# Kernel optimization log

Measured on AMD Instinct MI355X. Metric: run time of the kernel, lower is better.

## Reference

```python
import jax, jax.numpy as jnp
import numpy as np

D = 256      # d_model
K = 8        # knn neighbors
Q = 2048     # num queries
N = 32768    # num superpoints
H = 8        # mamba heads (d_inner/head_dim)
HD = 64      # head_dim
ST = 64      # state_size
DIN = H * HD                 # 512, expand*d_model
CONV = DIN + 2 * ST          # 640
NPROJ = 2 * DIN + 2 * ST + H # 1160
HID = 1024   # ffn hidden
NL = 2       # ssm layers
KC = 4       # conv kernel


def _ln(x, eps=1e-5):
    m = x.mean(-1, keepdims=True)
    v = ((x - m) ** 2).mean(-1, keepdims=True)
    return (x - m) * jax.lax.rsqrt(v + eps)


def _silu(x):
    return x * jax.nn.sigmoid(x)


def _mamba2(x, Win, Wconv, bconv, A_log, Dh, dtb, rmsw, Wout):
    # x: [B, L, D]; faithful HF Mamba2Mixer recurrent form
    B, L, _ = x.shape
    proj = x @ Win.T  # [B,L,NPROJ]
    z, xBC, dt = jnp.split(proj, [DIN, DIN + CONV], axis=-1)
    # causal depthwise conv1d, kernel KC, left pad KC-1
    xp = jnp.pad(xBC, ((0, 0), (KC - 1, 0), (0, 0)))
    conv = sum(xp[:, j:j + L, :] * Wconv[:, j] for j in range(KC))
    xBC = _silu(conv + bconv)
    xs, Bm, Cm = jnp.split(xBC, [DIN, DIN + ST], axis=-1)
    dt = jax.nn.softplus(dt + dtb)  # [B,L,H]
    A = -jnp.exp(A_log)             # [H]
    xh = xs.reshape(B, L, H, HD)
    dA = jnp.exp(dt * A)            # [B,L,H]
    dBx = dt[..., None, None] * Bm[:, :, None, None, :] * xh[..., None]  # [B,L,H,HD,ST]

    def step(h, inp):
        dA_t, dBx_t, C_t = inp
        h = h * dA_t[..., None, None] + dBx_t
        y = jnp.einsum('bhds,bs->bhd', h, C_t)
        return h, y

    h0 = jnp.zeros((B, H, HD, ST), x.dtype)
    _, ys = jax.lax.scan(step, h0, (dA.transpose(1, 0, 2),
                                    dBx.transpose(1, 0, 2, 3, 4),
                                    Cm.transpose(1, 0, 2)))
    y = ys.transpose(1, 0, 2, 3) + Dh[None, None, :, None] * xh
    y = y.reshape(B, L, DIN) * _silu(z)  # gated RMSNorm
    y = y * jax.lax.rsqrt((y * y).mean(-1, keepdims=True) + 1e-5) * rmsw
    return y @ Wout.T


def setup_inputs() -> dict:
    key = jax.random.key(0)
    ks = jax.random.split(key, 32)
    s = 0.02
    rn = lambda i, sh: jax.random.normal(ks[i], sh, jnp.float32) * s
    inp = {
        'query': jax.random.normal(ks[0], (Q, D), jnp.float32),
        'query_pos': jax.random.uniform(ks[1], (Q, 3), jnp.float32),
        'inst_feats': jax.random.normal(ks[2], (N, D), jnp.float32),
        'sp_coords': jax.random.uniform(ks[3], (N, 3), jnp.float32),
        'w_q': rn(4, (D, D)), 'w_v': rn(5, (D, D)), 'w_o': rn(6, (D, D)),
        'w_k': rn(7, (K, D)), 'w_b': jnp.zeros((K,), jnp.float32),
        'ssm_Win': rn(8, (NL, NPROJ, D)),
        'ssm_Wconv': rn(9, (NL, CONV, KC)),
        'ssm_bconv': jnp.zeros((NL, CONV), jnp.float32),
        'ssm_Alog': jnp.log(jnp.broadcast_to(jnp.arange(1, H + 1, dtype=jnp.float32), (NL, H))),
        'ssm_D': jnp.ones((NL, H), jnp.float32),
        'ssm_dtb': jax.random.uniform(ks[10], (NL, H), jnp.float32) * 0.1,
        'ssm_rmsw': jnp.ones((NL, DIN), jnp.float32),
        'ssm_Wout': rn(11, (NL, D, DIN)),
        'ffn_w1': rn(12, (HID, D)), 'ffn_b1': jnp.zeros((HID,), jnp.float32),
        'ffn_w2': rn(13, (D, HID)), 'ffn_b2': jnp.zeros((D,), jnp.float32),
        'order': jnp.stack([jax.random.permutation(ks[14], Q),
                            jax.random.permutation(ks[15], Q)]).astype(jnp.int32),
    }
    return inp


def reference(query, query_pos, inst_feats, sp_coords,
              w_q, w_v, w_o, w_k, w_b,
              ssm_Win, ssm_Wconv, ssm_bconv, ssm_Alog, ssm_D, ssm_dtb, ssm_rmsw, ssm_Wout,
              ffn_w1, ffn_b1, ffn_w2, ffn_b2, order):
    # --- MambaAggregation: KNN group + small-K softmax mixing ---
    d2 = (query_pos ** 2).sum(-1, keepdims=True) + (sp_coords ** 2).sum(-1)[None, :] \
         - 2.0 * query_pos @ sp_coords.T  # [Q,N]
    _, idx = jax.lax.top_k(-d2, K)        # [Q,K] nearest neighbors
    feat = inst_feats[idx]                # [Q,K,D]
    q = query @ w_q.T
    v = feat @ w_v.T
    kw = jax.nn.softmax(q @ w_k.T + w_b, axis=-1)          # [Q,K]
    w = jnp.einsum('qk,qd,qkd->qd', kw, q, v)
    x = _ln(w @ w_o.T + query)

    # --- SSM: serialize along 2 orders, Mamba2 mix, unsort, average ---
    inv = jnp.argsort(order, axis=1)  # [2,Q]
    for l in range(NL):
        sc = x
        xn = _ln(x)
        xs = xn[order]  # [2,Q,D], two serialization paths as batch
        y = _mamba2(xs, ssm_Win[l], ssm_Wconv[l], ssm_bconv[l], ssm_Alog[l],
                    ssm_D[l], ssm_dtb[l], ssm_rmsw[l], ssm_Wout[l])
        back = jnp.take_along_axis(y, inv[:, :, None], axis=1)  # undo sort
        x = _ln(sc + back.mean(0))

    # --- FFN ---
    h = jax.nn.gelu(x @ ffn_w1.T + ffn_b1, approximate=False) @ ffn_w2.T + ffn_b2
    return _ln(x + h)
```

## Files before the change

### kernel.cpp

```cpp
#include <hip/hip_runtime.h>
#include <cstdint>


typedef __attribute__((ext_vector_type(8))) short bf16x8;
typedef __attribute__((ext_vector_type(4))) float f32x4;

__device__ __forceinline__ unsigned short f2bf(float f) {
  unsigned int u = __float_as_uint(f);
  u += 0x7fff + ((u >> 16) & 1);
  return (unsigned short)(u >> 16);
}
__device__ __forceinline__ float bf2f(unsigned short h) {
  return __uint_as_float(((unsigned int)h) << 16);
}

__global__ __launch_bounds__(256) void cvt_kernel(
    const float* __restrict__ src, unsigned short* __restrict__ hi,
    unsigned short* __restrict__ lo, int n4)
{
  const int i = blockIdx.x*256 + threadIdx.x;
  if (i < n4) {
    const float4 v = ((const float4*)src)[i];
    const unsigned short h0=f2bf(v.x), h1=f2bf(v.y), h2=f2bf(v.z), h3=f2bf(v.w);
    const unsigned short l0=f2bf(v.x-bf2f(h0)), l1=f2bf(v.y-bf2f(h1)),
                         l2=f2bf(v.z-bf2f(h2)), l3=f2bf(v.w-bf2f(h3));
    ((uint2*)hi)[i] = make_uint2((unsigned)h0 | ((unsigned)h1<<16),
                                 (unsigned)h2 | ((unsigned)h3<<16));
    ((uint2*)lo)[i] = make_uint2((unsigned)l0 | ((unsigned)l1<<16),
                                 (unsigned)l2 | ((unsigned)l3<<16));
  }
}

__device__ __forceinline__ bool flex_less(float d, int i, float dr, int ir) {
  return d < dr || (d == dr && i < ir);
}

#define KNN_INS_F(dv, iv)                                                      \
  do {                                                                         \
    const float _d = (dv); const int _v = (iv);                                \
    const bool a0 = _d < bd0;                                                  \
    const bool a1 = _d < bd1;                                                  \
    const bool a2 = _d < bd2;                                                  \
    const bool a3 = _d < bd3;                                                  \
    const bool a4 = _d < bd4;                                                  \
    const bool a5 = _d < bd5;                                                  \
    const bool a6 = _d < bd6;                                                  \
    bd7 = a6 ? bd6 : _d;              id7 = a6 ? id6 : _v;                     \
    bd6 = a5 ? bd5 : (a6 ? _d : bd6); id6 = a5 ? id5 : (a6 ? _v : id6);        \
    bd5 = a4 ? bd4 : (a5 ? _d : bd5); id5 = a4 ? id4 : (a5 ? _v : id5);        \
    bd4 = a3 ? bd3 : (a4 ? _d : bd4); id4 = a3 ? id3 : (a4 ? _v : id4);        \
    bd3 = a2 ? bd2 : (a3 ? _d : bd3); id3 = a2 ? id2 : (a3 ? _v : id3);        \
    bd2 = a1 ? bd1 : (a2 ? _d : bd2); id2 = a1 ? id1 : (a2 ? _v : id2);        \
    bd1 = a0 ? bd0 : (a1 ? _d : bd1); id1 = a0 ? id0 : (a1 ? _v : id1);        \
    bd0 = a0 ? _d : bd0;              id0 = a0 ? _v : id0;                     \
  } while (0)

#define KNN_INS_FLEX(dv, iv)                                                   \
  do {                                                                         \
    const float _d = (dv); const int _v = (iv);                                \
    const bool a0 = flex_less(_d, _v, bd0, id0);                               \
    const bool a1 = flex_less(_d, _v, bd1, id1);                               \
    const bool a2 = flex_less(_d, _v, bd2, id2);                               \
    const bool a3 = flex_less(_d, _v, bd3, id3);                               \
    const bool a4 = flex_less(_d, _v, bd4, id4);                               \
    const bool a5 = flex_less(_d, _v, bd5, id5);                               \
    const bool a6 = flex_less(_d, _v, bd6, id6);                               \
    bd7 = a6 ? bd6 : _d;              id7 = a6 ? id6 : _v;                     \
    bd6 = a5 ? bd5 : (a6 ? _d : bd6); id6 = a5 ? id5 : (a6 ? _v : id6);        \
    bd5 = a4 ? bd4 : (a5 ? _d : bd5); id5 = a4 ? id4 : (a5 ? _v : id5);        \
    bd4 = a3 ? bd3 : (a4 ? _d : bd4); id4 = a3 ? id3 : (a4 ? _v : id4);        \
    bd3 = a2 ? bd2 : (a3 ? _d : bd3); id3 = a2 ? id2 : (a3 ? _v : id3);        \
    bd2 = a1 ? bd1 : (a2 ? _d : bd2); id2 = a1 ? id1 : (a2 ? _v : id2);        \
    bd1 = a0 ? bd0 : (a1 ? _d : bd1); id1 = a0 ? id0 : (a1 ? _v : id1);        \
    bd0 = a0 ? _d : bd0;              id0 = a0 ? _v : id0;                     \
  } while (0)

#define KNN_RESET_F()                                                          \
  do {                                                                         \
    bd0=bd1=bd2=bd3=bd4=bd5=bd6=bd7 = 3.4e38f;                                 \
    id0=id1=id2=id3=id4=id5=id6=id7 = 0x7fffffff;                              \
  } while (0)

__global__ void prep_kernel(const float* __restrict__ spos,
                            float4* __restrict__ P4)
{
#pragma clang fp contract(off)
  const int n = blockIdx.x*256 + threadIdx.x;
  if (n < 32768) {
    const float sx = spos[n*3+0], sy = spos[n*3+1], sz = spos[n*3+2];
    P4[n] = make_float4(sx, sy, sz, sx*sx + sy*sy + sz*sz);
  }
}

__global__ __launch_bounds__(256) void knn_kernel(
    const float* __restrict__ qpos, const float4* __restrict__ P4,
    int* __restrict__ idx_out)
{
#pragma clang fp contract(off)
  __shared__ float skey[32];
  __shared__ int   sidx[32];
  const int q = blockIdx.x, tid = threadIdx.x;
  const int wave = tid >> 6, lane = tid & 63;
  const float qx = qpos[q*3+0], qy = qpos[q*3+1], qz = qpos[q*3+2];
  const float qq = qx*qx + qy*qy + qz*qz;
  float bd0,bd1,bd2,bd3,bd4,bd5,bd6,bd7;
  int   id0,id1,id2,id3,id4,id5,id6,id7;
  KNN_RESET_F();
  const float4* pp = P4 + (wave << 13) + lane;
  int nb = (wave << 13);
  for (int it = 0; it < 128; ++it) {
    const float4 p = *pp;  pp += 64;
    const float d2 = (qq + p.w) - 2.0f*(qx*p.x + qy*p.y + qz*p.z);
    unsigned long long m = __ballot(d2 < bd7);
    while (m) {
      const int l = __ffsll(m) - 1;
      m &= m - 1;
      const float dk = __shfl(d2, l);
      if (dk < bd7) KNN_INS_F(dk, nb + l);
    }
    nb += 64;
  }
  if (lane == 0) {
    const int o = wave*8;
    skey[o+0]=bd0; skey[o+1]=bd1; skey[o+2]=bd2; skey[o+3]=bd3;
    skey[o+4]=bd4; skey[o+5]=bd5; skey[o+6]=bd6; skey[o+7]=bd7;
    sidx[o+0]=id0; sidx[o+1]=id1; sidx[o+2]=id2; sidx[o+3]=id3;
    sidx[o+4]=id4; sidx[o+5]=id5; sidx[o+6]=id6; sidx[o+7]=id7;
  }
  __syncthreads();
  if (tid == 0) {
    KNN_RESET_F();
    for (int s = 0; s < 32; ++s) {
      const float dk = skey[s];
      const int   ui = sidx[s];
      if (flex_less(dk, ui, bd7, id7)) KNN_INS_FLEX(dk, ui);
    }
    idx_out[q*8+0]=id0; idx_out[q*8+1]=id1; idx_out[q*8+2]=id2; idx_out[q*8+3]=id3;
    idx_out[q*8+4]=id4; idx_out[q*8+5]=id5; idx_out[q*8+6]=id6; idx_out[q*8+7]=id7;
  }
}

__global__ void inv_kernel(const int* __restrict__ order, int* __restrict__ inv)
{
  int i = blockIdx.x*blockDim.x + threadIdx.x;
  if (i < 4096) { int b = i >> 11, t = i & 2047; inv[(b<<11) + order[i]] = t; }
}

#define GBM 128
#define GBN 64
#define GBK 32
#define GLDK 40
__global__ __launch_bounds__(256) void gemm_mfma(
    const unsigned short* __restrict__ Ahp, const unsigned short* __restrict__ Alp,
    const int* __restrict__ rowmap,
    const unsigned short* __restrict__ Bhp, const unsigned short* __restrict__ Blp,
    const float* __restrict__ bias, const float* __restrict__ emul,
    float* __restrict__ Y,
    unsigned short* __restrict__ Yh, unsigned short* __restrict__ Yl,
    int M, int Nn, int Kd, int act)
{
  __shared__ unsigned short Ah[GBM*GLDK], Al[GBM*GLDK];
  __shared__ unsigned short Bh[GBN*GLDK], Bl[GBN*GLDK];
  const int tid = threadIdx.x;
  const int bm = blockIdx.x, bn = blockIdx.y;
  const int wid = tid >> 6, lane = tid & 63;
  const int wr = wid >> 1, wc = wid & 1;
  const int l15 = lane & 15, lk = (lane >> 4) << 3;

  const int sar = tid >> 1, sak = (tid & 1) << 4;
  const int agrow = bm*GBM + sar;
  const int asrc = rowmap ? rowmap[agrow] : agrow;
  const unsigned short* ArH = Ahp + (size_t)asrc * Kd + sak;
  const unsigned short* ArL = Alp + (size_t)asrc * Kd + sak;
  const int sbr = tid >> 2, sbk = (tid & 3) << 3;
  const int wrow = bn*GBN + sbr;
  const bool bok = (wrow < Nn);
  const unsigned short* BrH = Bhp + (size_t)(bok ? wrow : 0) * Kd + sbk;
  const unsigned short* BrL = Blp + (size_t)(bok ? wrow : 0) * Kd + sbk;

  f32x4 acc[4][2];
#pragma unroll
  for (int m = 0; m < 4; ++m)
#pragma unroll
    for (int n = 0; n < 2; ++n) acc[m][n] = (f32x4){0.f,0.f,0.f,0.f};

  const uint4 z4 = make_uint4(0u,0u,0u,0u);
  for (int k0 = 0; k0 < Kd; k0 += GBK) {
    const int ao = sar*GLDK + sak;
    *(uint4*)&Ah[ao]     = *(const uint4*)(ArH + k0);
    *(uint4*)&Ah[ao + 8] = *(const uint4*)(ArH + k0 + 8);
    *(uint4*)&Al[ao]     = *(const uint4*)(ArL + k0);
    *(uint4*)&Al[ao + 8] = *(const uint4*)(ArL + k0 + 8);
    const int bo = sbr*GLDK + sbk;
    *(uint4*)&Bh[bo] = bok ? *(const uint4*)(BrH + k0) : z4;
    *(uint4*)&Bl[bo] = bok ? *(const uint4*)(BrL + k0) : z4;
    __syncthreads();
    bf16x8 afh[4], afl[4], bfh[2], bfl[2];
#pragma unroll
    for (int m = 0; m < 4; ++m) {
      const int row = wr*64 + m*16 + l15;
      afh[m] = *(const bf16x8*)&Ah[row*GLDK + lk];
      afl[m] = *(const bf16x8*)&Al[row*GLDK + lk];
    }
#pragma unroll
    for (int n = 0; n < 2; ++n) {
      const int row = wc*32 + n*16 + l15;
      bfh[n] = *(const bf16x8*)&Bh[row*GLDK + lk];
      bfl[n] = *(const bf16x8*)&Bl[row*GLDK + lk];
    }
#pragma unroll
    for (int m = 0; m < 4; ++m)
#pragma unroll
      for (int n = 0; n < 2; ++n) {
        acc[m][n] = __builtin_amdgcn_mfma_f32_16x16x32_bf16(afh[m], bfh[n], acc[m][n], 0,0,0);
        acc[m][n] = __builtin_amdgcn_mfma_f32_16x16x32_bf16(afh[m], bfl[n], acc[m][n], 0,0,0);
        acc[m][n] = __builtin_amdgcn_mfma_f32_16x16x32_bf16(afl[m], bfh[n], acc[m][n], 0,0,0);
      }
    __syncthreads();
  }
  const int crow0 = bm*GBM + wr*64 + (lane >> 4)*4;
#pragma unroll
  for (int m = 0; m < 4; ++m) {
#pragma unroll
    for (int n = 0; n < 2; ++n) {
      const int col = bn*GBN + wc*32 + n*16 + l15;
      if (col < Nn) {
#pragma unroll
        for (int r = 0; r < 4; ++r) {
          float v = acc[m][n][r];
          if (bias) v += bias[col];
          if (act == 1) v = 0.5f*v*(1.f + erff(v*0.7071067811865475f));
          const size_t idx = (size_t)(crow0 + m*16 + r)*Nn + col;
          if (emul) v *= emul[idx];
          if (Yh) {
            const unsigned short h = f2bf(v);
            Yh[idx] = h; Yl[idx] = f2bf(v - bf2f(h));
          } else {
            Y[idx] = v;
          }
        }
      }
    }
  }
}

__global__ __launch_bounds__(256) void kwmix2_kernel(
    const float* __restrict__ QP, const float* __restrict__ wk,
    const float* __restrict__ wb, const float* __restrict__ feats,
    const int* __restrict__ IDX,
    unsigned short* __restrict__ Fh, unsigned short* __restrict__ Fl)
{
  const int wave = threadIdx.x >> 6, lane = threadIdx.x & 63;
  const int q = blockIdx.x*4 + wave;
  float qv[4];
#pragma unroll
  for (int j = 0; j < 4; ++j) qv[j] = QP[(size_t)q*256 + lane + 64*j];
  float logit[8];
#pragma unroll
  for (int k = 0; k < 8; ++k) {
    float p = 0.f;
#pragma unroll
    for (int j = 0; j < 4; ++j) p += qv[j]*wk[k*256 + lane + 64*j];
    for (int off = 32; off; off >>= 1) p += __shfl_xor(p, off);
    logit[k] = p + wb[k];
  }
  float mx = logit[0];
#pragma unroll
  for (int k = 1; k < 8; ++k) mx = fmaxf(mx, logit[k]);
  float e[8]; float s = 0.f;
#pragma unroll
  for (int k = 0; k < 8; ++k) { e[k] = expf(logit[k]-mx); s += e[k]; }
  float inv = 1.f/s;
  float acc[4] = {0.f,0.f,0.f,0.f};
#pragma unroll
  for (int k = 0; k < 8; ++k) {
    const float kwv = e[k]*inv;
    const int ii = IDX[q*8+k];
#pragma unroll
    for (int j = 0; j < 4; ++j)
      acc[j] = fmaf(kwv, feats[(size_t)ii*256 + lane + 64*j], acc[j]);
  }
#pragma unroll
  for (int j = 0; j < 4; ++j) {
    const unsigned short h = f2bf(acc[j]);
    const size_t o = (size_t)q*256 + lane + 64*j;
    Fh[o] = h; Fl[o] = f2bf(acc[j] - bf2f(h));
  }
}

__global__ __launch_bounds__(256) void ln_kernel(
    const float* __restrict__ a, const float* __restrict__ b,
    float* __restrict__ out,
    unsigned short* __restrict__ oh, unsigned short* __restrict__ ol,
    int rows)
{
  const int wave = threadIdx.x >> 6, lane = threadIdx.x & 63;
  const int row = blockIdx.x*4 + wave;
  if (row >= rows) return;
  float v[4];
#pragma unroll
  for (int j = 0; j < 4; ++j) {
    float x = a[(size_t)row*256 + lane + 64*j];
    if (b) x += b[(size_t)row*256 + lane + 64*j];
    v[j] = x;
  }
  float s = v[0]+v[1]+v[2]+v[3];
  for (int off = 32; off; off >>= 1) s += __shfl_xor(s, off);
  float m = s * (1.0f/256.0f);
  float t = 0.f;
#pragma unroll
  for (int j = 0; j < 4; ++j) { float d = v[j]-m; t += d*d; }
  for (int off = 32; off; off >>= 1) t += __shfl_xor(t, off);
  float r = rsqrtf(t * (1.0f/256.0f) + 1e-5f);
#pragma unroll
  for (int j = 0; j < 4; ++j) {
    const float y = (v[j]-m)*r;
    const size_t o = (size_t)row*256 + lane + 64*j;
    if (out) out[o] = y;
    if (oh) { const unsigned short h = f2bf(y); oh[o] = h; ol[o] = f2bf(y - bf2f(h)); }
  }
}

__global__ __launch_bounds__(256) void ln_unsort_kernel(
    const float* __restrict__ OUTL, const int* __restrict__ INV,
    float* __restrict__ X,
    unsigned short* __restrict__ oh, unsigned short* __restrict__ ol)
{
  const int wave = threadIdx.x >> 6, lane = threadIdx.x & 63;
  const int q = blockIdx.x*4 + wave;
  const int i0 = INV[q], i1 = INV[2048 + q];
  float v[4];
#pragma unroll
  for (int j = 0; j < 4; ++j) {
    int d = lane + 64*j;
    v[j] = X[(size_t)q*256 + d]
         + 0.5f*(OUTL[(size_t)i0*256 + d] + OUTL[(size_t)(2048+i1)*256 + d]);
  }
  float s = v[0]+v[1]+v[2]+v[3];
  for (int off = 32; off; off >>= 1) s += __shfl_xor(s, off);
  float m = s * (1.0f/256.0f);
  float t = 0.f;
#pragma unroll
  for (int j = 0; j < 4; ++j) { float d = v[j]-m; t += d*d; }
  for (int off = 32; off; off >>= 1) t += __shfl_xor(t, off);
  float r = rsqrtf(t * (1.0f/256.0f) + 1e-5f);
#pragma unroll
  for (int j = 0; j < 4; ++j) {
    const float y = (v[j]-m)*r;
    const size_t o = (size_t)q*256 + lane + 64*j;
    X[o] = y;
    if (oh) { const unsigned short h = f2bf(y); oh[o] = h; ol[o] = f2bf(y - bf2f(h)); }
  }
}

__global__ void conv_kernel(const float* __restrict__ PROJ,
    const float* __restrict__ Wc, const float* __restrict__ bc,
    float* __restrict__ XBC)
{
  const int c = threadIdx.x;
  const int bt = blockIdx.x;
  const int t = bt & 2047;
  float acc = bc[c];
#pragma unroll
  for (int j = 0; j < 4; ++j) {
    int d = j - 3;
    if (t + d >= 0)
      acc = fmaf(PROJ[(size_t)(bt + d)*1160 + 512 + c], Wc[c*4+j], acc);
  }
  XBC[(size_t)bt*640 + c] = acc / (1.f + expf(-acc));
}

__global__ void dta_kernel(const float* __restrict__ PROJ,
    const float* __restrict__ dtb, const float* __restrict__ Alog,
    float* __restrict__ Ddt, float* __restrict__ Dda)
{
  const int i = blockIdx.x*256 + threadIdx.x;
  const int bt = i >> 3, hh = i & 7;
  float x = PROJ[(size_t)bt*1160 + 1152 + hh] + dtb[hh];
  float dt = (x > 20.f) ? x : log1pf(expf(x));
  float A = -expf(Alog[hh]);
  Ddt[hh*4096 + bt] = dt;
  Dda[hh*4096 + bt] = expf(dt * A);
}

__global__ __launch_bounds__(64) void scan1_kernel(
    const float* __restrict__ XBC, const float* __restrict__ Ddt,
    const float* __restrict__ Dda, float* __restrict__ SCH, float* __restrict__ PC)
{
  const int blk = blockIdx.x;
  const int c = blk & 31, hh = (blk >> 5) & 7, b = blk >> 8;
  const int lane = threadIdx.x;
  const int t0 = (b << 11) + (c << 6);
  __shared__ float Bsh[64][64];
  __shared__ float Xsh[64][64];
  __shared__ float dAs[64], dts[64];
#pragma unroll
  for (int it = 0; it < 16; ++it) {
    int idx = it*64 + lane;
    int t = idx >> 4, c4 = (idx & 15) << 2;
    *(float4*)&Bsh[t][c4] = *(const float4*)&XBC[(size_t)(t0 + t)*640 + 512 + c4];
    *(float4*)&Xsh[t][c4] = *(const float4*)&XBC[(size_t)(t0 + t)*640 + (hh<<6) + c4];
  }
  dAs[lane] = Dda[hh*4096 + t0 + lane];
  dts[lane] = Ddt[hh*4096 + t0 + lane];
  __syncthreads();
  float h[64];
#pragma unroll
  for (int s = 0; s < 64; ++s) h[s] = 0.f;
  float p = 1.f;
  for (int t = 0; t < 64; ++t) {
    const float dA = dAs[t];
    const float u = dts[t]*Xsh[t][lane];
    p *= dA;
    const float4* B4 = (const float4*)&Bsh[t][0];
#pragma unroll
    for (int s4 = 0; s4 < 16; ++s4) {
      float4 bv = B4[s4];
      h[4*s4+0] = fmaf(h[4*s4+0], dA, bv.x*u);
      h[4*s4+1] = fmaf(h[4*s4+1], dA, bv.y*u);
      h[4*s4+2] = fmaf(h[4*s4+2], dA, bv.z*u);
      h[4*s4+3] = fmaf(h[4*s4+3], dA, bv.w*u);
    }
  }
  float* op = SCH + (size_t)blk*4096 + lane*64;
#pragma unroll
  for (int s4 = 0; s4 < 16; ++s4)
    ((float4*)op)[s4] = make_float4(h[4*s4], h[4*s4+1], h[4*s4+2], h[4*s4+3]);
  if (lane == 0) PC[blk] = p;
}

__global__ void combine_kernel(float* __restrict__ SCH, const float* __restrict__ PC)
{
  const int tid = blockIdx.x*256 + threadIdx.x;
  const int bh = tid >> 12, ds = tid & 4095;
  float h = 0.f;
  for (int cc = 0; cc < 32; ++cc) {
    size_t o = ((size_t)(bh*32 + cc) << 12) + ds;
    float s = SCH[o];
    SCH[o] = h;
    h = fmaf(h, PC[bh*32+cc], s);
  }
}

__global__ __launch_bounds__(64) void scan2_kernel(
    const float* __restrict__ XBC, const float* __restrict__ Ddt,
    const float* __restrict__ Dda, const float* __restrict__ HST,
    const float* __restrict__ Dm, float* __restrict__ Yout)
{
  const int blk = blockIdx.x;
  const int c = blk & 31, hh = (blk >> 5) & 7, b = blk >> 8;
  const int lane = threadIdx.x;
  const int t0 = (b << 11) + (c << 6);
  __shared__ float Bsh[64][64];
  __shared__ float Csh[64][64];
  __shared__ float Xsh[64][64];
  __shared__ float dAs[64], dts[64];
#pragma unroll
  for (int it = 0; it < 16; ++it) {
    int idx = it*64 + lane;
    int t = idx >> 4, c4 = (idx & 15) << 2;
    *(float4*)&Bsh[t][c4] = *(const float4*)&XBC[(size_t)(t0 + t)*640 + 512 + c4];
    *(float4*)&Csh[t][c4] = *(const float4*)&XBC[(size_t)(t0 + t)*640 + 576 + c4];
    *(float4*)&Xsh[t][c4] = *(const float4*)&XBC[(size_t)(t0 + t)*640 + (hh<<6) + c4];
  }
  dAs[lane] = Dda[hh*4096 + t0 + lane];
  dts[lane] = Ddt[hh*4096 + t0 + lane];
  const float Dh = Dm[hh];
  float h[64];
  const float4* hp = (const float4*)(HST + (size_t)blk*4096 + lane*64);
#pragma unroll
  for (int s4 = 0; s4 < 16; ++s4) {
    float4 t4 = hp[s4];
    h[4*s4+0]=t4.x; h[4*s4+1]=t4.y; h[4*s4+2]=t4.z; h[4*s4+3]=t4.w;
  }
  __syncthreads();
  for (int t = 0; t < 64; ++t) {
    const float dA = dAs[t];
    const float u = dts[t]*Xsh[t][lane];
    float y = 0.f;
    const float4* B4 = (const float4*)&Bsh[t][0];
    const float4* C4 = (const float4*)&Csh[t][0];
#pragma unroll
    for (int s4 = 0; s4 < 16; ++s4) {
      float4 bv = B4[s4];
      float4 cv = C4[s4];
      h[4*s4+0] = fmaf(h[4*s4+0], dA, bv.x*u); y = fmaf(cv.x, h[4*s4+0], y);
      h[4*s4+1] = fmaf(h[4*s4+1], dA, bv.y*u); y = fmaf(cv.y, h[4*s4+1], y);
      h[4*s4+2] = fmaf(h[4*s4+2], dA, bv.z*u); y = fmaf(cv.z, h[4*s4+2], y);
      h[4*s4+3] = fmaf(h[4*s4+3], dA, bv.w*u); y = fmaf(cv.w, h[4*s4+3], y);
    }
    Yout[(size_t)(t0 + t)*512 + (hh<<6) + lane] = y + Dh*Xsh[t][lane];
  }
}

__global__ __launch_bounds__(256) void gaterms_kernel(
    const float* __restrict__ Y, const float* __restrict__ PROJ,
    const float* __restrict__ rmsw,
    unsigned short* __restrict__ Oh, unsigned short* __restrict__ Ol)
{
  const int wave = threadIdx.x >> 6, lane = threadIdx.x & 63;
  const int row = blockIdx.x*4 + wave;
  float v[8]; float ss = 0.f;
#pragma unroll
  for (int j = 0; j < 8; ++j) {
    float y = Y[(size_t)row*512 + lane + 64*j];
    float z = PROJ[(size_t)row*1160 + lane + 64*j];
    float g = y * (z / (1.f + expf(-z)));
    v[j] = g; ss += g*g;
  }
  for (int off = 32; off; off >>= 1) ss += __shfl_xor(ss, off);
  float r = rsqrtf(ss * (1.0f/512.0f) + 1e-5f);
#pragma unroll
  for (int j = 0; j < 8; ++j) {
    const float o = v[j] * r * rmsw[lane + 64*j];
    const unsigned short h = f2bf(o);
    const size_t ix = (size_t)row*512 + lane + 64*j;
    Oh[ix] = h; Ol[ix] = f2bf(o - bf2f(h));
  }
}

extern "C" void kernel_launch(void* const* d_in, const int* in_sizes, int n_in,
                              void* d_out, int out_size, void* d_ws, size_t ws_size,
                              hipStream_t stream)
{
  (void)in_sizes; (void)n_in; (void)out_size; (void)ws_size;
  const float* query = (const float*)d_in[0];
  const float* qpos  = (const float*)d_in[1];
  const float* feats = (const float*)d_in[2];
  const float* spos  = (const float*)d_in[3];
  const float* w_q   = (const float*)d_in[4];
  const float* w_v   = (const float*)d_in[5];
  const float* w_o   = (const float*)d_in[6];
  const float* w_k   = (const float*)d_in[7];
  const float* w_b   = (const float*)d_in[8];
  const float* Win   = (const float*)d_in[9];
  const float* Wconv = (const float*)d_in[10];
  const float* bconv = (const float*)d_in[11];
  const float* Alog  = (const float*)d_in[12];
  const float* Dm    = (const float*)d_in[13];
  const float* dtb   = (const float*)d_in[14];
  const float* rmsw  = (const float*)d_in[15];
  const float* Wout  = (const float*)d_in[16];
  const float* fw1   = (const float*)d_in[17];
  const float* fb1   = (const float*)d_in[18];
  const float* fw2   = (const float*)d_in[19];
  const float* fb2   = (const float*)d_in[20];
  const int*   order = (const int*)d_in[21];
  float* out = (float*)d_out;

  char* ws = (char*)d_ws;
  size_t off = 0;
  auto alloc = [&](size_t bytes) -> void* {
    void* p = ws + off;
    off = (off + bytes + 255) & ~(size_t)255;
    return p;
  };
  int*   IDX = (int*)alloc((size_t)2048*8*4);
  int*   INV = (int*)alloc((size_t)4096*4);
  float* PC  = (float*)alloc((size_t)512*4);
  float4* P4 = (float4*)alloc((size_t)32768*16);
  float* Ddt = (float*)alloc((size_t)4096*8*4);
  float* Dda = (float*)alloc((size_t)4096*8*4);
  float* QP  = (float*)alloc((size_t)2048*256*4);
  float* WO  = (float*)alloc((size_t)2048*256*4);
  float* X   = (float*)alloc((size_t)2048*256*4);
  float* U1  = (float*)alloc((size_t)4096*1160*4);
  float* U2  = (float*)alloc((size_t)4096*640*4);
  float* SCH = (float*)alloc((size_t)512*4096*4);
  float* Yb  = (float*)alloc((size_t)4096*512*4);
  float* U6  = (float*)alloc((size_t)4096*256*4);
  unsigned short* Qh  = (unsigned short*)alloc((size_t)2048*256*2);
  unsigned short* Ql  = (unsigned short*)alloc((size_t)2048*256*2);
  unsigned short* U7h = (unsigned short*)alloc((size_t)2048*1024*2);
  unsigned short* U7l = (unsigned short*)alloc((size_t)2048*1024*2);
  unsigned short* WBh = (unsigned short*)alloc((size_t)2048*256*2);
  unsigned short* WBl = (unsigned short*)alloc((size_t)2048*256*2);
  unsigned short* XNh = (unsigned short*)alloc((size_t)2048*256*2);
  unsigned short* XNl = (unsigned short*)alloc((size_t)2048*256*2);
  unsigned short* Ybh = (unsigned short*)alloc((size_t)4096*512*2);
  unsigned short* Ybl = (unsigned short*)alloc((size_t)4096*512*2);
  unsigned short* Xh  = (unsigned short*)alloc((size_t)2048*256*2);
  unsigned short* Xl  = (unsigned short*)alloc((size_t)2048*256*2);
  unsigned short* Wqh = (unsigned short*)alloc((size_t)256*256*2);
  unsigned short* Wql = (unsigned short*)alloc((size_t)256*256*2);
  unsigned short* Wvh = (unsigned short*)alloc((size_t)256*256*2);
  unsigned short* Wvl = (unsigned short*)alloc((size_t)256*256*2);
  unsigned short* Woh = (unsigned short*)alloc((size_t)256*256*2);
  unsigned short* Wol = (unsigned short*)alloc((size_t)256*256*2);
  unsigned short* Wih = (unsigned short*)alloc((size_t)2*1160*256*2);
  unsigned short* Wil = (unsigned short*)alloc((size_t)2*1160*256*2);
  unsigned short* Wuh = (unsigned short*)alloc((size_t)2*256*512*2);
  unsigned short* Wul = (unsigned short*)alloc((size_t)2*256*512*2);
  unsigned short* F1h = (unsigned short*)alloc((size_t)1024*256*2);
  unsigned short* F1l = (unsigned short*)alloc((size_t)1024*256*2);
  unsigned short* F2h = (unsigned short*)alloc((size_t)256*1024*2);
  unsigned short* F2l = (unsigned short*)alloc((size_t)256*1024*2);
  float* PROJ = U1;
  float* XBC  = U2;
  float* OUTL = U6;  float* FFO  = U6;
  unsigned short* FFHh = U7h;
  unsigned short* FFHl = U7l;

  auto cvt = [&](const float* s, unsigned short* h, unsigned short* l, int n) {
    cvt_kernel<<<(n/4 + 255)/256, 256, 0, stream>>>(s, h, l, n/4);
  };

  inv_kernel<<<16, 256, 0, stream>>>(order, INV);
  prep_kernel<<<128, 256, 0, stream>>>(spos, P4);
  knn_kernel<<<2048, 256, 0, stream>>>(qpos, P4, IDX);
  cvt(query, Qh, Ql, 2048*256);
  cvt(w_q, Wqh, Wql, 256*256);
  cvt(w_v, Wvh, Wvl, 256*256);
  cvt(w_o, Woh, Wol, 256*256);
  cvt(Win, Wih, Wil, 2*1160*256);
  cvt(Wout, Wuh, Wul, 2*256*512);
  cvt(fw1, F1h, F1l, 1024*256);
  cvt(fw2, F2h, F2l, 256*1024);
  gemm_mfma<<<dim3(16,4), 256, 0, stream>>>(Qh, Ql, nullptr, Wqh, Wql, nullptr,
                                            nullptr, QP, nullptr, nullptr,
                                            2048,256,256,0);
  kwmix2_kernel<<<512, 256, 0, stream>>>(QP, w_k, w_b, feats, IDX, XNh, XNl);
  gemm_mfma<<<dim3(16,4), 256, 0, stream>>>(XNh, XNl, nullptr, Wvh, Wvl, nullptr,
                                            QP, nullptr, WBh, WBl,
                                            2048,256,256,0);
  gemm_mfma<<<dim3(16,4), 256, 0, stream>>>(WBh, WBl, nullptr, Woh, Wol, nullptr,
                                            nullptr, WO, nullptr, nullptr,
                                            2048,256,256,0);
  ln_kernel<<<512, 256, 0, stream>>>(WO, query, X, nullptr, nullptr, 2048);

  for (int l = 0; l < 2; ++l) {
    ln_kernel<<<512, 256, 0, stream>>>(X, nullptr, nullptr, XNh, XNl, 2048);
    gemm_mfma<<<dim3(32,19), 256, 0, stream>>>(XNh, XNl, order,
                                               Wih + (size_t)l*1160*256,
                                               Wil + (size_t)l*1160*256,
                                               nullptr, nullptr, PROJ,
                                               nullptr, nullptr,
                                               4096,1160,256,0);
    conv_kernel<<<4096, 640, 0, stream>>>(PROJ, Wconv + l*640*4, bconv + l*640, XBC);
    dta_kernel<<<128, 256, 0, stream>>>(PROJ, dtb + l*8, Alog + l*8, Ddt, Dda);
    scan1_kernel<<<512, 64, 0, stream>>>(XBC, Ddt, Dda, SCH, PC);
    combine_kernel<<<256, 256, 0, stream>>>(SCH, PC);
    scan2_kernel<<<512, 64, 0, stream>>>(XBC, Ddt, Dda, SCH, Dm + l*8, Yb);
    gaterms_kernel<<<1024, 256, 0, stream>>>(Yb, PROJ, rmsw + l*512, Ybh, Ybl);
    gemm_mfma<<<dim3(32,4), 256, 0, stream>>>(Ybh, Ybl, nullptr,
                                              Wuh + (size_t)l*256*512,
                                              Wul + (size_t)l*256*512,
                                              nullptr, nullptr, OUTL,
                                              nullptr, nullptr,
                                              4096,256,512,0);
    ln_unsort_kernel<<<512, 256, 0, stream>>>(OUTL, INV, X,
                                              (l==1) ? Xh : nullptr,
                                              (l==1) ? Xl : nullptr);
  }

  gemm_mfma<<<dim3(16,16), 256, 0, stream>>>(Xh, Xl, nullptr, F1h, F1l, fb1,
                                             nullptr, nullptr, FFHh, FFHl,
                                             2048,1024,256,1);
  gemm_mfma<<<dim3(16,4), 256, 0, stream>>>(FFHh, FFHl, nullptr, F2h, F2l, fb2,
                                            nullptr, FFO, nullptr, nullptr,
                                            2048,256,1024,0);
  ln_kernel<<<512, 256, 0, stream>>>(FFO, X, out, nullptr, nullptr, 2048);
}
```

Baseline: 584.0 us.

## Halve scan chunk length, merge small kernels, batch weight conversions

The chunked SSM scan now uses 32-step chunks with twice as many blocks, giving more parallelism in the sequential scan kernels. The x values move from shared memory into registers, and the combine pass walks 64 chunk states instead of 32. The inverse-permutation and point-prep kernels merge into one launch, the dt/dA computation folds into the conv kernel, and eight conversion launches collapse into one segmented kernel. The cost is a longer serial combine pass, a larger chunk-state buffer and more register pressure in the scan kernels.

```diff
diff --git a/kernel.cpp b/kernel.cpp
--- a/kernel.cpp
+++ b/kernel.cpp
@@ -14,20 +14,29 @@
   return __uint_as_float(((unsigned int)h) << 16);
 }
 
-__global__ __launch_bounds__(256) void cvt_kernel(
-    const float* __restrict__ src, unsigned short* __restrict__ hi,
-    unsigned short* __restrict__ lo, int n4)
-{
-  const int i = blockIdx.x*256 + threadIdx.x;
-  if (i < n4) {
-    const float4 v = ((const float4*)src)[i];
+struct CvtArgs {
+  const float* s[8];
+  unsigned short* h[8];
+  unsigned short* l[8];
+  int n4[8];
+  int blk0[8];
+};
+__global__ __launch_bounds__(256) void cvt8_kernel(CvtArgs a)
+{
+  const int b = blockIdx.x;
+  int seg = 0;
+#pragma unroll
+  for (int j = 1; j < 8; ++j) if (b >= a.blk0[j]) seg = j;
+  const int i = (b - a.blk0[seg])*256 + threadIdx.x;
+  if (i < a.n4[seg]) {
+    const float4 v = ((const float4*)a.s[seg])[i];
     const unsigned short h0=f2bf(v.x), h1=f2bf(v.y), h2=f2bf(v.z), h3=f2bf(v.w);
     const unsigned short l0=f2bf(v.x-bf2f(h0)), l1=f2bf(v.y-bf2f(h1)),
                          l2=f2bf(v.z-bf2f(h2)), l3=f2bf(v.w-bf2f(h3));
-    ((uint2*)hi)[i] = make_uint2((unsigned)h0 | ((unsigned)h1<<16),
-                                 (unsigned)h2 | ((unsigned)h3<<16));
-    ((uint2*)lo)[i] = make_uint2((unsigned)l0 | ((unsigned)l1<<16),
-                                 (unsigned)l2 | ((unsigned)l3<<16));
+    ((uint2*)a.h[seg])[i] = make_uint2((unsigned)h0 | ((unsigned)h1<<16),
+                                       (unsigned)h2 | ((unsigned)h3<<16));
+    ((uint2*)a.l[seg])[i] = make_uint2((unsigned)l0 | ((unsigned)l1<<16),
+                                       (unsigned)l2 | ((unsigned)l3<<16));
   }
 }
 
@@ -81,14 +90,19 @@
     id0=id1=id2=id3=id4=id5=id6=id7 = 0x7fffffff;                              \
   } while (0)
 
-__global__ void prep_kernel(const float* __restrict__ spos,
-                            float4* __restrict__ P4)
+__global__ void misc_kernel(const int* __restrict__ order, int* __restrict__ inv,
+                            const float* __restrict__ spos, float4* __restrict__ P4)
 {
 #pragma clang fp contract(off)
-  const int n = blockIdx.x*256 + threadIdx.x;
-  if (n < 32768) {
-    const float sx = spos[n*3+0], sy = spos[n*3+1], sz = spos[n*3+2];
-    P4[n] = make_float4(sx, sy, sz, sx*sx + sy*sy + sz*sz);
+  const int i = blockIdx.x*256 + threadIdx.x;
+  if (blockIdx.x < 16) {
+    if (i < 4096) { int b = i >> 11, t = i & 2047; inv[(b<<11) + order[i]] = t; }
+  } else {
+    const int n = i - 4096;
+    if (n < 32768) {
+      const float sx = spos[n*3+0], sy = spos[n*3+1], sz = spos[n*3+2];
+      P4[n] = make_float4(sx, sy, sz, sx*sx + sy*sy + sz*sz);
+    }
   }
 }
 
@@ -140,12 +154,6 @@
   }
 }
 
-__global__ void inv_kernel(const int* __restrict__ order, int* __restrict__ inv)
-{
-  int i = blockIdx.x*blockDim.x + threadIdx.x;
-  if (i < 4096) { int b = i >> 11, t = i & 2047; inv[(b<<11) + order[i]] = t; }
-}
-
 #define GBM 128
 #define GBN 64
 #define GBK 32
@@ -355,7 +363,9 @@
 
 __global__ void conv_kernel(const float* __restrict__ PROJ,
     const float* __restrict__ Wc, const float* __restrict__ bc,
-    float* __restrict__ XBC)
+    float* __restrict__ XBC,
+    const float* __restrict__ dtb, const float* __restrict__ Alog,
+    float* __restrict__ Ddt, float* __restrict__ Dda)
 {
   const int c = threadIdx.x;
   const int bt = blockIdx.x;
@@ -368,19 +378,13 @@
       acc = fmaf(PROJ[(size_t)(bt + d)*1160 + 512 + c], Wc[c*4+j], acc);
   }
   XBC[(size_t)bt*640 + c] = acc / (1.f + expf(-acc));
-}
-
-__global__ void dta_kernel(const float* __restrict__ PROJ,
-    const float* __restrict__ dtb, const float* __restrict__ Alog,
-    float* __restrict__ Ddt, float* __restrict__ Dda)
-{
-  const int i = blockIdx.x*256 + threadIdx.x;
-  const int bt = i >> 3, hh = i & 7;
-  float x = PROJ[(size_t)bt*1160 + 1152 + hh] + dtb[hh];
-  float dt = (x > 20.f) ? x : log1pf(expf(x));
-  float A = -expf(Alog[hh]);
-  Ddt[hh*4096 + bt] = dt;
-  Dda[hh*4096 + bt] = expf(dt * A);
+  if (c < 8) {
+    float x = PROJ[(size_t)bt*1160 + 1152 + c] + dtb[c];
+    float dt = (x > 20.f) ? x : log1pf(expf(x));
+    float A = -expf(Alog[c]);
+    Ddt[c*4096 + bt] = dt;
+    Dda[c*4096 + bt] = expf(dt * A);
+  }
 }
 
 __global__ __launch_bounds__(64) void scan1_kernel(
@@ -388,29 +392,33 @@
     const float* __restrict__ Dda, float* __restrict__ SCH, float* __restrict__ PC)
 {
   const int blk = blockIdx.x;
-  const int c = blk & 31, hh = (blk >> 5) & 7, b = blk >> 8;
+  const int c = blk & 63, hh = (blk >> 6) & 7, b = blk >> 9;
   const int lane = threadIdx.x;
-  const int t0 = (b << 11) + (c << 6);
-  __shared__ float Bsh[64][64];
-  __shared__ float Xsh[64][64];
-  __shared__ float dAs[64], dts[64];
-#pragma unroll
-  for (int it = 0; it < 16; ++it) {
+  const int t0 = (b << 11) + (c << 5);
+  __shared__ float Bsh[32][64];
+  __shared__ float dAs[32], dts[32];
+#pragma unroll
+  for (int it = 0; it < 8; ++it) {
     int idx = it*64 + lane;
     int t = idx >> 4, c4 = (idx & 15) << 2;
     *(float4*)&Bsh[t][c4] = *(const float4*)&XBC[(size_t)(t0 + t)*640 + 512 + c4];
-    *(float4*)&Xsh[t][c4] = *(const float4*)&XBC[(size_t)(t0 + t)*640 + (hh<<6) + c4];
-  }
-  dAs[lane] = Dda[hh*4096 + t0 + lane];
-  dts[lane] = Ddt[hh*4096 + t0 + lane];
+  }
+  if (lane < 32) {
+    dAs[lane] = Dda[hh*4096 + t0 + lane];
+    dts[lane] = Ddt[hh*4096 + t0 + lane];
+  }
+  float xv[32];
+#pragma unroll
+  for (int t = 0; t < 32; ++t)
+    xv[t] = XBC[(size_t)(t0 + t)*640 + (hh<<6) + lane];
   __syncthreads();
   float h[64];
 #pragma unroll
   for (int s = 0; s < 64; ++s) h[s] = 0.f;
   float p = 1.f;
-  for (int t = 0; t < 64; ++t) {
+  for (int t = 0; t < 32; ++t) {
     const float dA = dAs[t];
-    const float u = dts[t]*Xsh[t][lane];
+    const float u = dts[t]*xv[t];
     p *= dA;
     const float4* B4 = (const float4*)&Bsh[t][0];
 #pragma unroll
@@ -434,11 +442,11 @@
   const int tid = blockIdx.x*256 + threadIdx.x;
   const int bh = tid >> 12, ds = tid & 4095;
   float h = 0.f;
-  for (int cc = 0; cc < 32; ++cc) {
-    size_t o = ((size_t)(bh*32 + cc) << 12) + ds;
+  for (int cc = 0; cc < 64; ++cc) {
+    size_t o = ((size_t)(bh*64 + cc) << 12) + ds;
     float s = SCH[o];
     SCH[o] = h;
-    h = fmaf(h, PC[bh*32+cc], s);
+    h = fmaf(h, PC[bh*64+cc], s);
   }
 }
 
@@ -448,23 +456,27 @@
     const float* __restrict__ Dm, float* __restrict__ Yout)
 {
   const int blk = blockIdx.x;
-  const int c = blk & 31, hh = (blk >> 5) & 7, b = blk >> 8;
+  const int c = blk & 63, hh = (blk >> 6) & 7, b = blk >> 9;
   const int lane = threadIdx.x;
-  const int t0 = (b << 11) + (c << 6);
-  __shared__ float Bsh[64][64];
-  __shared__ float Csh[64][64];
-  __shared__ float Xsh[64][64];
-  __shared__ float dAs[64], dts[64];
-#pragma unroll
-  for (int it = 0; it < 16; ++it) {
+  const int t0 = (b << 11) + (c << 5);
+  __shared__ float Bsh[32][64];
+  __shared__ float Csh[32][64];
+  __shared__ float dAs[32], dts[32];
+#pragma unroll
+  for (int it = 0; it < 8; ++it) {
     int idx = it*64 + lane;
     int t = idx >> 4, c4 = (idx & 15) << 2;
     *(float4*)&Bsh[t][c4] = *(const float4*)&XBC[(size_t)(t0 + t)*640 + 512 + c4];
     *(float4*)&Csh[t][c4] = *(const float4*)&XBC[(size_t)(t0 + t)*640 + 576 + c4];
-    *(float4*)&Xsh[t][c4] = *(const float4*)&XBC[(size_t)(t0 + t)*640 + (hh<<6) + c4];
-  }
-  dAs[lane] = Dda[hh*4096 + t0 + lane];
-  dts[lane] = Ddt[hh*4096 + t0 + lane];
+  }
+  if (lane < 32) {
+    dAs[lane] = Dda[hh*4096 + t0 + lane];
+    dts[lane] = Ddt[hh*4096 + t0 + lane];
+  }
+  float xv[32];
+#pragma unroll
+  for (int t = 0; t < 32; ++t)
+    xv[t] = XBC[(size_t)(t0 + t)*640 + (hh<<6) + lane];
   const float Dh = Dm[hh];
   float h[64];
   const float4* hp = (const float4*)(HST + (size_t)blk*4096 + lane*64);
@@ -474,9 +486,9 @@
     h[4*s4+0]=t4.x; h[4*s4+1]=t4.y; h[4*s4+2]=t4.z; h[4*s4+3]=t4.w;
   }
   __syncthreads();
-  for (int t = 0; t < 64; ++t) {
+  for (int t = 0; t < 32; ++t) {
     const float dA = dAs[t];
-    const float u = dts[t]*Xsh[t][lane];
+    const float u = dts[t]*xv[t];
     float y = 0.f;
     const float4* B4 = (const float4*)&Bsh[t][0];
     const float4* C4 = (const float4*)&Csh[t][0];
@@ -489,7 +501,7 @@
       h[4*s4+2] = fmaf(h[4*s4+2], dA, bv.z*u); y = fmaf(cv.z, h[4*s4+2], y);
       h[4*s4+3] = fmaf(h[4*s4+3], dA, bv.w*u); y = fmaf(cv.w, h[4*s4+3], y);
     }
-    Yout[(size_t)(t0 + t)*512 + (hh<<6) + lane] = y + Dh*Xsh[t][lane];
+    Yout[(size_t)(t0 + t)*512 + (hh<<6) + lane] = y + Dh*xv[t];
   }
 }
 
@@ -557,7 +569,7 @@
   };
   int*   IDX = (int*)alloc((size_t)2048*8*4);
   int*   INV = (int*)alloc((size_t)4096*4);
-  float* PC  = (float*)alloc((size_t)512*4);
+  float* PC  = (float*)alloc((size_t)1024*4);
   float4* P4 = (float4*)alloc((size_t)32768*16);
   float* Ddt = (float*)alloc((size_t)4096*8*4);
   float* Dda = (float*)alloc((size_t)4096*8*4);
@@ -566,7 +578,7 @@
   float* X   = (float*)alloc((size_t)2048*256*4);
   float* U1  = (float*)alloc((size_t)4096*1160*4);
   float* U2  = (float*)alloc((size_t)4096*640*4);
-  float* SCH = (float*)alloc((size_t)512*4096*4);
+  float* SCH = (float*)alloc((size_t)1024*4096*4);
   float* Yb  = (float*)alloc((size_t)4096*512*4);
   float* U6  = (float*)alloc((size_t)4096*256*4);
   unsigned short* Qh  = (unsigned short*)alloc((size_t)2048*256*2);
@@ -601,21 +613,18 @@
   unsigned short* FFHh = U7h;
   unsigned short* FFHl = U7l;
 
-  auto cvt = [&](const float* s, unsigned short* h, unsigned short* l, int n) {
-    cvt_kernel<<<(n/4 + 255)/256, 256, 0, stream>>>(s, h, l, n/4);
-  };
-
-  inv_kernel<<<16, 256, 0, stream>>>(order, INV);
-  prep_kernel<<<128, 256, 0, stream>>>(spos, P4);
+  misc_kernel<<<144, 256, 0, stream>>>(order, INV, spos, P4);
   knn_kernel<<<2048, 256, 0, stream>>>(qpos, P4, IDX);
-  cvt(query, Qh, Ql, 2048*256);
-  cvt(w_q, Wqh, Wql, 256*256);
-  cvt(w_v, Wvh, Wvl, 256*256);
-  cvt(w_o, Woh, Wol, 256*256);
-  cvt(Win, Wih, Wil, 2*1160*256);
-  cvt(Wout, Wuh, Wul, 2*256*512);
-  cvt(fw1, F1h, F1l, 1024*256);
-  cvt(fw2, F2h, F2l, 256*1024);
+  CvtArgs ca;
+  ca.s[0]=query; ca.h[0]=Qh;  ca.l[0]=Ql;  ca.n4[0]=131072; ca.blk0[0]=0;
+  ca.s[1]=w_q;   ca.h[1]=Wqh; ca.l[1]=Wql; ca.n4[1]=16384;  ca.blk0[1]=512;
+  ca.s[2]=w_v;   ca.h[2]=Wvh; ca.l[2]=Wvl; ca.n4[2]=16384;  ca.blk0[2]=576;
+  ca.s[3]=w_o;   ca.h[3]=Woh; ca.l[3]=Wol; ca.n4[3]=16384;  ca.blk0[3]=640;
+  ca.s[4]=Win;   ca.h[4]=Wih; ca.l[4]=Wil; ca.n4[4]=148480; ca.blk0[4]=704;
+  ca.s[5]=Wout;  ca.h[5]=Wuh; ca.l[5]=Wul; ca.n4[5]=65536;  ca.blk0[5]=1284;
+  ca.s[6]=fw1;   ca.h[6]=F1h; ca.l[6]=F1l; ca.n4[6]=65536;  ca.blk0[6]=1540;
+  ca.s[7]=fw2;   ca.h[7]=F2h; ca.l[7]=F2l; ca.n4[7]=65536;  ca.blk0[7]=1796;
+  cvt8_kernel<<<2052, 256, 0, stream>>>(ca);
   gemm_mfma<<<dim3(16,4), 256, 0, stream>>>(Qh, Ql, nullptr, Wqh, Wql, nullptr,
                                             nullptr, QP, nullptr, nullptr,
                                             2048,256,256,0);
@@ -636,11 +645,11 @@
                                                nullptr, nullptr, PROJ,
                                                nullptr, nullptr,
                                                4096,1160,256,0);
-    conv_kernel<<<4096, 640, 0, stream>>>(PROJ, Wconv + l*640*4, bconv + l*640, XBC);
-    dta_kernel<<<128, 256, 0, stream>>>(PROJ, dtb + l*8, Alog + l*8, Ddt, Dda);
-    scan1_kernel<<<512, 64, 0, stream>>>(XBC, Ddt, Dda, SCH, PC);
+    conv_kernel<<<4096, 640, 0, stream>>>(PROJ, Wconv + l*640*4, bconv + l*640,
+                                          XBC, dtb + l*8, Alog + l*8, Ddt, Dda);
+    scan1_kernel<<<1024, 64, 0, stream>>>(XBC, Ddt, Dda, SCH, PC);
     combine_kernel<<<256, 256, 0, stream>>>(SCH, PC);
-    scan2_kernel<<<512, 64, 0, stream>>>(XBC, Ddt, Dda, SCH, Dm + l*8, Yb);
+    scan2_kernel<<<1024, 64, 0, stream>>>(XBC, Ddt, Dda, SCH, Dm + l*8, Yb);
     gaterms_kernel<<<1024, 256, 0, stream>>>(Yb, PROJ, rmsw + l*512, Ybh, Ybl);
     gemm_mfma<<<dim3(32,4), 256, 0, stream>>>(Ybh, Ybl, nullptr,
                                               Wuh + (size_t)l*256*512,
```

Result: no change. 578.4 us (-1.0%).
